# Kernel tuning notes

Hardware: AMD Instinct MI355X
Metric: run time of the kernel (lower is better)

The kernel has to match this reference:

```python
import jax, jax.numpy as jnp
import numpy as np

B, N = 16, 4096
N_IN, E_OUT = 128, 128          # inpt_dim[1], outp_dim[0]
OUT_N = 128                     # outp_dim[1]
G_DIM, CTXT_DIM = 64, 64
NODE_IN = E_OUT + N_IN          # 256, pre_ln size
CTXT_IN = G_DIM + CTXT_DIM      # 128
HID_F, HID_A = 256, 128
N_HEADS = 4
HEAD_DIM = OUT_N // N_HEADS     # 32
LN_EPS = 1e-5


def _init_w(key, fan_in, fan_out):
    return jax.random.normal(key, (fan_in, fan_out), jnp.float32) / np.float32(np.sqrt(fan_in))


def setup_inputs() -> dict:
    key = jax.random.key(0)
    ks = jax.random.split(key, 10)
    nodes = jax.random.normal(ks[0], (B, N, N_IN), jnp.float32)
    pooled_edges = jax.random.normal(ks[1], (B, N, E_OUT), jnp.float32)
    # variable-length graphs: valid prefix per graph (at least half the nodes)
    lengths = jax.random.randint(ks[2], (B,), N // 2, N + 1)
    mask = jnp.arange(N)[None, :] < lengths[:, None]
    globs = jax.random.normal(ks[3], (B, G_DIM), jnp.float32)
    ctxt = jax.random.normal(ks[4], (B, CTXT_DIM), jnp.float32)
    return {
        "nodes": nodes,
        "pooled_edges": pooled_edges,
        "mask": mask,
        "globs": globs,
        "ctxt": ctxt,
        "ln_g": jnp.ones((NODE_IN,), jnp.float32),
        "ln_b": jnp.zeros((NODE_IN,), jnp.float32),
        "feat_w1": _init_w(ks[5], NODE_IN + CTXT_IN, HID_F),
        "feat_b1": jnp.zeros((HID_F,), jnp.float32),
        "feat_w2": _init_w(ks[6], HID_F, OUT_N),
        "feat_b2": jnp.zeros((OUT_N,), jnp.float32),
        "attn_w1": _init_w(ks[7], NODE_IN + CTXT_IN, HID_A),
        "attn_b1": jnp.zeros((HID_A,), jnp.float32),
        "attn_w2": _init_w(ks[8], HID_A, N_HEADS),
        "attn_b2": jnp.zeros((N_HEADS,), jnp.float32),
    }


def _mlp(x, w1, b1, w2, b2):
    # DenseNetwork: one hidden block with LeakyReLU ("lrlu"), linear output
    h = jax.nn.leaky_relu(x @ w1 + b1)
    return h @ w2 + b2


def reference(nodes, pooled_edges, mask, globs, ctxt, ln_g, ln_b,
              feat_w1, feat_b1, feat_w2, feat_b2,
              attn_w1, attn_b1, attn_w2, attn_b2):
    # nodes = cat([graph.nodes, pooled_edges]) -> pre-LayerNorm
    x = jnp.concatenate([nodes, pooled_edges], axis=-1)           # [B,N,256]
    mu = jnp.mean(x, axis=-1, keepdims=True)
    var = jnp.var(x, axis=-1, keepdims=True)
    x = (x - mu) * jax.lax.rsqrt(var + LN_EPS) * ln_g + ln_b

    # high-level context broadcast to every node
    hl = jnp.concatenate([globs, ctxt], axis=-1)                   # [B,128]
    hl = jnp.broadcast_to(hl[:, None, :], (x.shape[0], x.shape[1], hl.shape[-1]))
    xin = jnp.concatenate([x, hl], axis=-1)                        # [B,N,384]

    # attention net with -inf padding, softmax over node axis (dim=-2)
    logits = _mlp(xin, attn_w1, attn_b1, attn_w2, attn_b2)          # [B,N,H]
    logits = jnp.where(mask[..., None], logits, -jnp.inf)
    w = jax.nn.softmax(logits, axis=1) / np.float32(np.sqrt(OUT_N))
    w = jnp.where(mask[..., None], w, 0.0)

    # feature net with 0 padding + residual (same_size)
    feats = _mlp(xin, feat_w1, feat_b1, feat_w2, feat_b2)           # [B,N,128]
    feats = jnp.where(mask[..., None], feats, 0.0)
    new_nodes = feats + nodes

    # expand per-head weights across head_dim, flatten, weighted node pooling
    w_full = jnp.repeat(w, HEAD_DIM, axis=-1)                       # [B,N,128]
    pooled = jnp.sum(new_nodes * w_full, axis=1)                    # [B,128]
    return (new_nodes, pooled)
```

## Files before the change

kernel.cpp:

```cpp
#include <hip/hip_runtime.h>
#include <stdint.h>

typedef unsigned short u16;
typedef unsigned char  u8;
typedef unsigned int   u32;
typedef __attribute__((ext_vector_type(8))) short bf16x8;
typedef __attribute__((ext_vector_type(4))) float f32x4;

static __device__ __forceinline__ float bf2f(u32 u) {
    union { u32 i; float f; } x; x.i = u << 16; return x.f;
}
static __device__ __forceinline__ u16 f2bf(float f) {
    union { u32 i; float f; } x; x.f = f;
    return (u16)((x.i + 0x7fffu + ((x.i >> 16) & 1u)) >> 16);
}
static __device__ __forceinline__ u32 packbf(float a, float b) {
    return (u32)f2bf(a) | ((u32)f2bf(b) << 16);
}
static __device__ __forceinline__ float ldf(const void* p, int i, int isf32) {
    return isf32 ? ((const float*)p)[i] : bf2f(((const u16*)p)[i]);
}
static __device__ __forceinline__ bool mvalid(const void* mask, int g, int mi32) {
    return mi32 ? (((const int*)mask)[g] != 0) : (((const u8*)mask)[g] != 0);
}

#define NTOT 65536
#define SXLD 264
#define SHLD 136

#define BAR() do { asm volatile("s_waitcnt lgkmcnt(0)" ::: "memory"); \
                   __builtin_amdgcn_s_barrier();                      \
                   asm volatile("" ::: "memory"); } while (0)

__global__ __launch_bounds__(256) void k0_prep(
    const void* __restrict__ feat_w1, const void* __restrict__ attn_w1,
    const void* __restrict__ feat_b1, const void* __restrict__ attn_b1,
    const void* __restrict__ feat_w2, const void* __restrict__ attn_w2,
    const void* __restrict__ globs, const void* __restrict__ ctxt,
    const void* __restrict__ ln_g,
    u16* __restrict__ W1t, u16* __restrict__ W2t, u16* __restrict__ aw2t,
    float* __restrict__ hlc)
{
    __shared__ u16 tile[64][66];
    __shared__ float hl[128];
    const int isf32 = (((const u32*)ln_g)[0] == 0x3F800000u);
    const int bid = blockIdx.x;
    const int t = threadIdx.x;

    if (bid < 24) {
        int jt = bid >> 2, kt = bid & 3;
        int j0 = jt * 64, k0 = kt * 64;
        int jj = t & 63, kq = t >> 6;
#pragma unroll
        for (int r = 0; r < 16; r++) {
            int kk = r * 4 + kq;
            int j = j0 + jj;
            float v = (j < 256) ? ldf(feat_w1, (k0 + kk) * 256 + j, isf32)
                                : ldf(attn_w1, (k0 + kk) * 128 + (j - 256), isf32);
            tile[kk][jj] = f2bf(v);
        }
        __syncthreads();
        int kk2 = t & 63, jq = t >> 6;
#pragma unroll
        for (int r = 0; r < 16; r++) {
            int jj2 = r * 4 + jq;
            W1t[(size_t)(j0 + jj2) * 256 + k0 + kk2] = tile[kk2][jj2];
        }
    } else if (bid < 32) {
        int id2 = bid - 24;
        int ct2 = id2 >> 2, kt = id2 & 3;
        int c0 = ct2 * 64, k0 = kt * 64;
        int cc = t & 63, kq = t >> 6;
#pragma unroll
        for (int r = 0; r < 16; r++) {
            int kk = r * 4 + kq;
            tile[kk][cc] = f2bf(ldf(feat_w2, (k0 + kk) * 128 + c0 + cc, isf32));
        }
        __syncthreads();
        int kk2 = t & 63, cq = t >> 6;
#pragma unroll
        for (int r = 0; r < 16; r++) {
            int cc2 = r * 4 + cq;
            W2t[(size_t)(c0 + cc2) * 256 + k0 + kk2] = tile[kk2][cc2];
        }
    } else if (bid == 32) {
#pragma unroll
        for (int i = 0; i < 8; i++) {
            int e = i * 256 + t;
            int n = e >> 7, k = e & 127;
            aw2t[e] = (n < 4) ? f2bf(ldf(attn_w2, k * 4 + n, isf32)) : (u16)0;
        }
    } else {
        int b = bid - 33;
        if (t < 64)       hl[t] = ldf(globs, b * 64 + t, isf32);
        else if (t < 128) hl[t] = ldf(ctxt, b * 64 + (t - 64), isf32);
        __syncthreads();
        {
            float s = ldf(feat_b1, t, isf32);
#pragma unroll 8
            for (int c = 0; c < 128; c++)
                s += hl[c] * ldf(feat_w1, (256 + c) * 256 + t, isf32);
            hlc[b * 384 + t] = s;
        }
        if (t < 128) {
            float s = ldf(attn_b1, t, isf32);
#pragma unroll 8
            for (int c = 0; c < 128; c++)
                s += hl[c] * ldf(attn_w1, (256 + c) * 128 + t, isf32);
            hlc[b * 384 + 256 + t] = s;
        }
    }
}

__global__ __launch_bounds__(256, 4) void k_mega(
    const void* __restrict__ nodes, const void* __restrict__ edges,
    const void* __restrict__ ln_g, const void* __restrict__ ln_b,
    const u16* __restrict__ W1t, const u16* __restrict__ W2t,
    const u16* __restrict__ aw2t, const float* __restrict__ hlc,
    const void* __restrict__ attn_b2, const void* __restrict__ feat_b2,
    const void* __restrict__ mask,
    float* __restrict__ logits, void* __restrict__ outp)
{
    __shared__ __align__(16) u16 sX[32 * SXLD];
    __shared__ __align__(16) u16 sH[2][32 * SHLD];
    __shared__ float sG[256], sBt[256];
    const int t = threadIdx.x;
    const int isf32 = (((const u32*)ln_g)[0] == 0x3F800000u);
    const int mi32  = (((const u32*)mask)[0] == 1u);
    const int r = t >> 3, q8 = t & 7;
    const int g00 = blockIdx.x * 64;
    const int g01 = g00 + 32;

    sG[t]  = ldf(ln_g, t, isf32);
    sBt[t] = ldf(ln_b, t, isf32);

    float4 f0a[4], f0b[4], f1a[4];
    uint4  u0[4],  u1[4];
    if (isf32) {
#pragma unroll
        for (int j = 0; j < 4; j++) {
            int c = q8 + j * 8;
            const float* s0 = (c < 16)
                ? ((const float*)nodes + (size_t)(g00 + r) * 128 + c * 8)
                : ((const float*)edges + (size_t)(g00 + r) * 128 + (c - 16) * 8);
            f0a[j] = ((const float4*)s0)[0];
            f0b[j] = ((const float4*)s0)[1];
        }
#pragma unroll
        for (int j = 0; j < 4; j++) {
            int c = q8 + j * 8;
            const float* s1 = (c < 16)
                ? ((const float*)nodes + (size_t)(g01 + r) * 128 + c * 8)
                : ((const float*)edges + (size_t)(g01 + r) * 128 + (c - 16) * 8);
            f1a[j] = ((const float4*)s1)[0];
        }
    } else {
#pragma unroll
        for (int j = 0; j < 4; j++) {
            int c = q8 + j * 8;
            const u16* s0 = (c < 16)
                ? ((const u16*)nodes + (size_t)(g00 + r) * 128 + c * 8)
                : ((const u16*)edges + (size_t)(g00 + r) * 128 + (c - 16) * 8);
            u0[j] = ((const uint4*)s0)[0];
        }
#pragma unroll
        for (int j = 0; j < 4; j++) {
            int c = q8 + j * 8;
            const u16* s1 = (c < 16)
                ? ((const u16*)nodes + (size_t)(g01 + r) * 128 + c * 8)
                : ((const u16*)edges + (size_t)(g01 + r) * 128 + (c - 16) * 8);
            u1[j] = ((const uint4*)s1)[0];
        }
    }
    BAR();

    u32 pk[16];

    auto ln_to_sX = [&]() {
        float s = 0.f, q = 0.f;
#pragma unroll
        for (int i = 0; i < 16; i++) {
            float lo = bf2f(pk[i] & 0xffffu), hi = bf2f(pk[i] >> 16);
            s += lo + hi; q += lo * lo + hi * hi;
        }
        s += __shfl_xor(s, 1, 64); s += __shfl_xor(s, 2, 64); s += __shfl_xor(s, 4, 64);
        q += __shfl_xor(q, 1, 64); q += __shfl_xor(q, 2, 64); q += __shfl_xor(q, 4, 64);
        float mu = s * (1.f / 256.f);
        float var = q * (1.f / 256.f) - mu * mu;
        float rs = rsqrtf(var + 1e-5f);
#pragma unroll
        for (int j = 0; j < 4; j++) {
            int c = q8 + j * 8;
            u32 ow[4];
#pragma unroll
            for (int k2 = 0; k2 < 4; k2++) {
                int col = c * 8 + k2 * 2;
                u32 w2 = pk[4 * j + k2];
                float y0 = (bf2f(w2 & 0xffffu) - mu) * rs * sG[col]     + sBt[col];
                float y1 = (bf2f(w2 >> 16)     - mu) * rs * sG[col + 1] + sBt[col + 1];
                ow[k2] = packbf(y0, y1);
            }
            *(uint4*)&sX[r * SXLD + c * 8] = make_uint4(ow[0], ow[1], ow[2], ow[3]);
        }
    };

    if (isf32) {
#pragma unroll
        for (int j = 0; j < 4; j++) {
            pk[4 * j]     = packbf(f0a[j].x, f0a[j].y);
            pk[4 * j + 1] = packbf(f0a[j].z, f0a[j].w);
            pk[4 * j + 2] = packbf(f0b[j].x, f0b[j].y);
            pk[4 * j + 3] = packbf(f0b[j].z, f0b[j].w);
        }
    } else {
#pragma unroll
        for (int j = 0; j < 4; j++) {
            pk[4 * j] = u0[j].x; pk[4 * j + 1] = u0[j].y;
            pk[4 * j + 2] = u0[j].z; pk[4 * j + 3] = u0[j].w;
        }
    }
    ln_to_sX();
    BAR();

    const int w = t >> 6, l = t & 63;
    const int lr = l & 15, lq = l >> 4;

    auto do_tile = [&](int g0) {
        const int b = g0 >> 12;
        f32x4 acc2[2][2];
#pragma unroll
        for (int rt = 0; rt < 2; rt++)
#pragma unroll
            for (int ct = 0; ct < 2; ct++) acc2[rt][ct] = (f32x4){0.f, 0.f, 0.f, 0.f};

        const int order[3] = {2, 0, 1};
#pragma unroll
        for (int oi = 0; oi < 3; oi++) {
            const int nt = order[oi];
            u16* sHc = &sH[oi & 1][0];

            float hbv[2];
#pragma unroll
            for (int ct = 0; ct < 2; ct++)
                hbv[ct] = hlc[b * 384 + nt * 128 + w * 32 + ct * 16 + lr];

            f32x4 acc1[2][2];
#pragma unroll
            for (int rt = 0; rt < 2; rt++)
#pragma unroll
                for (int ct = 0; ct < 2; ct++) acc1[rt][ct] = (f32x4){0.f, 0.f, 0.f, 0.f};

            const u16* Wp = W1t + (size_t)(nt * 128 + w * 32 + lr) * 256;
#pragma unroll
            for (int kh = 0; kh < 2; kh++) {
                bf16x8 bW[4][2];
#pragma unroll
                for (int kk = 0; kk < 4; kk++)
#pragma unroll
                    for (int ct = 0; ct < 2; ct++)
                        bW[kk][ct] = *(const bf16x8*)(Wp + ct * 16 * 256 + (kh * 4 + kk) * 32 + lq * 8);
#pragma unroll
                for (int kk = 0; kk < 4; kk++) {
                    bf16x8 aF[2];
#pragma unroll
                    for (int rt = 0; rt < 2; rt++)
                        aF[rt] = *(const bf16x8*)&sX[(rt * 16 + lr) * SXLD + ((kh * 4 + kk) * 4 + lq) * 8];
#pragma unroll
                    for (int rt = 0; rt < 2; rt++)
#pragma unroll
                        for (int ct = 0; ct < 2; ct++)
                            acc1[rt][ct] = __builtin_amdgcn_mfma_f32_16x16x32_bf16(aF[rt], bW[kk][ct], acc1[rt][ct], 0, 0, 0);
                }
            }

#pragma unroll
            for (int rt = 0; rt < 2; rt++)
#pragma unroll
                for (int ct = 0; ct < 2; ct++)
#pragma unroll
                    for (int reg = 0; reg < 4; reg++) {
                        int row = rt * 16 + lq * 4 + reg;
                        int col = w * 32 + ct * 16 + lr;
                        float hv = acc1[rt][ct][reg] + hbv[ct];
                        hv = (hv >= 0.f) ? hv : 0.01f * hv;
                        sHc[row * SHLD + col] = f2bf(hv);
                    }
            BAR();

            if (nt == 2) {
                if (w < 2) {
                    f32x4 accL = (f32x4){0.f, 0.f, 0.f, 0.f};
#pragma unroll
                    for (int kk = 0; kk < 4; kk++) {
                        bf16x8 aF = *(const bf16x8*)&sHc[(w * 16 + lr) * SHLD + (kk * 4 + lq) * 8];
                        bf16x8 bF = *(const bf16x8*)(aw2t + lr * 128 + kk * 32 + lq * 8);
                        accL = __builtin_amdgcn_mfma_f32_16x16x32_bf16(aF, bF, accL, 0, 0, 0);
                    }
                    if (lr < 4) {
                        float bias = ldf(attn_b2, lr, isf32);
#pragma unroll
                        for (int reg = 0; reg < 4; reg++) {
                            int row = g0 + w * 16 + lq * 4 + reg;
                            logits[(size_t)lr * NTOT + row] = accL[reg] + bias;
                        }
                    }
                }
            } else {
                const u16* W2p = W2t + (size_t)(w * 32 + lr) * 256 + nt * 128;
                bf16x8 bW2[4][2];
#pragma unroll
                for (int kk = 0; kk < 4; kk++)
#pragma unroll
                    for (int ct = 0; ct < 2; ct++)
                        bW2[kk][ct] = *(const bf16x8*)(W2p + ct * 16 * 256 + kk * 32 + lq * 8);
#pragma unroll
                for (int kk = 0; kk < 4; kk++) {
                    bf16x8 aF[2];
#pragma unroll
                    for (int rt = 0; rt < 2; rt++)
                        aF[rt] = *(const bf16x8*)&sHc[(rt * 16 + lr) * SHLD + (kk * 4 + lq) * 8];
#pragma unroll
                    for (int rt = 0; rt < 2; rt++)
#pragma unroll
                        for (int ct = 0; ct < 2; ct++)
                            acc2[rt][ct] = __builtin_amdgcn_mfma_f32_16x16x32_bf16(aF[rt], bW2[kk][ct], acc2[rt][ct], 0, 0, 0);
                }
            }
        }

#pragma unroll
        for (int rt = 0; rt < 2; rt++)
#pragma unroll
            for (int ct = 0; ct < 2; ct++)
#pragma unroll
                for (int reg = 0; reg < 4; reg++) {
                    int row = rt * 16 + lq * 4 + reg;
                    int col = w * 32 + ct * 16 + lr;
                    int g = g0 + row;
                    float v = acc2[rt][ct][reg] + ldf(feat_b2, col, isf32);
                    v = mvalid(mask, g, mi32) ? v : 0.f;
                    v += ldf(nodes, g * 128 + col, isf32);
                    size_t idx = (size_t)g * 128 + col;
                    if (isf32) ((float*)outp)[idx] = v;
                    else       ((u16*)outp)[idx] = f2bf(v);
                }
    };

    do_tile(g00);

    if (isf32) {
#pragma unroll
        for (int j = 0; j < 4; j++) {
            int c = q8 + j * 8;
            const float* s1 = (c < 16)
                ? ((const float*)nodes + (size_t)(g01 + r) * 128 + c * 8)
                : ((const float*)edges + (size_t)(g01 + r) * 128 + (c - 16) * 8);
            float4 fb = ((const float4*)s1)[1];
            pk[4 * j]     = packbf(f1a[j].x, f1a[j].y);
            pk[4 * j + 1] = packbf(f1a[j].z, f1a[j].w);
            pk[4 * j + 2] = packbf(fb.x, fb.y);
            pk[4 * j + 3] = packbf(fb.z, fb.w);
        }
    } else {
#pragma unroll
        for (int j = 0; j < 4; j++) {
            pk[4 * j] = u1[j].x; pk[4 * j + 1] = u1[j].y;
            pk[4 * j + 2] = u1[j].z; pk[4 * j + 3] = u1[j].w;
        }
    }
    ln_to_sX();
    BAR();

    do_tile(g01);
}

__global__ __launch_bounds__(1024) void k_softmax(
    const float* __restrict__ logits, const void* __restrict__ mask,
    const void* __restrict__ ln_g,
    float* __restrict__ wbuf, float* __restrict__ pooled)
{
    __shared__ float red[32];
    const int bh = blockIdx.x;
    const int b = bh >> 2, h = bh & 3;
    const int t = threadIdx.x;
    const int mi32 = (((const u32*)mask)[0] == 1u);
    if (t < 32) pooled[bh * 32 + t] = 0.f;

    float4 lg = ((const float4*)(logits + (size_t)h * NTOT + b * 4096))[t];
    int v0, v1, v2, v3;
    if (mi32) {
        int4 m4 = ((const int4*)mask)[b * 1024 + t];
        v0 = m4.x; v1 = m4.y; v2 = m4.z; v3 = m4.w;
    } else {
        u32 mb = ((const u32*)mask)[b * 1024 + t];
        v0 = mb & 255; v1 = (mb >> 8) & 255; v2 = (mb >> 16) & 255; v3 = mb >> 24;
    }
    float mx = -1e30f;
    if (v0) mx = lg.x;
    if (v1) mx = fmaxf(mx, lg.y);
    if (v2) mx = fmaxf(mx, lg.z);
    if (v3) mx = fmaxf(mx, lg.w);
#pragma unroll
    for (int o = 1; o < 64; o <<= 1) mx = fmaxf(mx, __shfl_xor(mx, o, 64));
    if ((t & 63) == 0) red[t >> 6] = mx;
    __syncthreads();
    float m2 = red[0];
#pragma unroll
    for (int i = 1; i < 16; i++) m2 = fmaxf(m2, red[i]);
    float e0 = v0 ? expf(lg.x - m2) : 0.f;
    float e1 = v1 ? expf(lg.y - m2) : 0.f;
    float e2 = v2 ? expf(lg.z - m2) : 0.f;
    float e3 = v3 ? expf(lg.w - m2) : 0.f;
    float sv = e0 + e1 + e2 + e3;
#pragma unroll
    for (int o = 1; o < 64; o <<= 1) sv += __shfl_xor(sv, o, 64);
    __syncthreads();
    if ((t & 63) == 0) red[16 + (t >> 6)] = sv;
    __syncthreads();
    float s2 = 0.f;
#pragma unroll
    for (int i = 0; i < 16; i++) s2 += red[16 + i];
    float inv = 0.08838834764831845f / s2;
    float4 o4 = make_float4(e0 * inv, e1 * inv, e2 * inv, e3 * inv);
    ((float4*)(wbuf + (size_t)h * NTOT + b * 4096))[t] = o4;
}

__global__ __launch_bounds__(256) void k_pool(
    const void* __restrict__ outp, const float* __restrict__ wbuf,
    const void* __restrict__ ln_g, float* __restrict__ pooled)
{
    __shared__ float sW[4][32];
    __shared__ float pacc[8][128];
    const int blk = blockIdx.x;
    const int b = blk >> 7, s = blk & 127;
    const int t = threadIdx.x;
    const int isf32 = (((const u32*)ln_g)[0] == 0x3F800000u);

    if (t < 128) {
        int h = t >> 5, n = t & 31;
        sW[h][n] = wbuf[(size_t)h * NTOT + b * 4096 + s * 32 + n];
    }
    __syncthreads();

    const int c4 = (t & 31) * 4, r8 = t >> 5;
    const int h = c4 >> 5;
    const size_t rowbase = (size_t)(b * 4096 + s * 32);
    float a0 = 0.f, a1 = 0.f, a2 = 0.f, a3 = 0.f;
    if (isf32) {
        const float* op = (const float*)outp;
#pragma unroll
        for (int i = 0; i < 4; i++) {
            int row = i * 8 + r8;
            float4 v = *(const float4*)(op + (rowbase + row) * 128 + c4);
            float wv = sW[h][row];
            a0 += v.x * wv; a1 += v.y * wv; a2 += v.z * wv; a3 += v.w * wv;
        }
    } else {
        const u16* op = (const u16*)outp;
#pragma unroll
        for (int i = 0; i < 4; i++) {
            int row = i * 8 + r8;
            uint2 v = *(const uint2*)(op + (rowbase + row) * 128 + c4);
            float wv = sW[h][row];
            a0 += bf2f(v.x & 0xffffu) * wv; a1 += bf2f(v.x >> 16) * wv;
            a2 += bf2f(v.y & 0xffffu) * wv; a3 += bf2f(v.y >> 16) * wv;
        }
    }
    *(float4*)&pacc[r8][c4] = make_float4(a0, a1, a2, a3);
    __syncthreads();
    if (t < 128) {
        float sum = 0.f;
#pragma unroll
        for (int r = 0; r < 8; r++) sum += pacc[r][t];
        atomicAdd(&pooled[b * 128 + t], sum);
    }
}

__global__ __launch_bounds__(256) void k_fin(const float* __restrict__ pooled,
                                             const void* __restrict__ ln_g,
                                             void* __restrict__ outbase)
{
    int t = blockIdx.x * 256 + threadIdx.x;
    const int isf32 = (((const u32*)ln_g)[0] == 0x3F800000u);
    if (t < 2048) {
        size_t off = (size_t)NTOT * 128 + t;
        if (isf32) ((float*)outbase)[off] = pooled[t];
        else       ((u16*)outbase)[off] = f2bf(pooled[t]);
    }
}

extern "C" void kernel_launch(void* const* d_in, const int* in_sizes, int n_in,
                              void* d_out, int out_size, void* d_ws, size_t ws_size,
                              hipStream_t stream)
{
    const void* nodes   = d_in[0];
    const void* edges   = d_in[1];
    const void* mask    = d_in[2];
    const void* globs   = d_in[3];
    const void* ctxt    = d_in[4];
    const void* ln_g    = d_in[5];
    const void* ln_b    = d_in[6];
    const void* feat_w1 = d_in[7];
    const void* feat_b1 = d_in[8];
    const void* feat_w2 = d_in[9];
    const void* feat_b2 = d_in[10];
    const void* attn_w1 = d_in[11];
    const void* attn_b1 = d_in[12];
    const void* attn_w2 = d_in[13];
    const void* attn_b2 = d_in[14];

    char* ws = (char*)d_ws;
    u16*   W1t    = (u16*)ws;   ws += (size_t)384 * 256 * 2;
    u16*   W2t    = (u16*)ws;   ws += (size_t)128 * 256 * 2;
    u16*   aw2t   = (u16*)ws;   ws += (size_t)16 * 128 * 2;
    float* hlc    = (float*)ws; ws += (size_t)16 * 384 * 4;
    float* logits = (float*)ws; ws += (size_t)NTOT * 4 * 4;
    float* wbuf   = (float*)ws; ws += (size_t)NTOT * 4 * 4;
    float* pooled = (float*)ws; ws += (size_t)2048 * 4;

    k0_prep  <<<dim3(49),   dim3(256),  0, stream>>>(feat_w1, attn_w1, feat_b1, attn_b1,
                                                     feat_w2, attn_w2, globs, ctxt, ln_g,
                                                     W1t, W2t, aw2t, hlc);
    k_mega   <<<dim3(1024), dim3(256),  0, stream>>>(nodes, edges, ln_g, ln_b, W1t, W2t,
                                                     aw2t, hlc, attn_b2, feat_b2, mask,
                                                     logits, d_out);
    k_softmax<<<dim3(64),   dim3(1024), 0, stream>>>(logits, mask, ln_g, wbuf, pooled);
    k_pool   <<<dim3(2048), dim3(256),  0, stream>>>(d_out, wbuf, ln_g, pooled);
    k_fin    <<<dim3(8),    dim3(256),  0, stream>>>(pooled, ln_g, d_out);
}
```

Baseline: 242.1 us.

## Stage feature-MLP output through LDS for coalesced residual add and stores

The epilogue now writes the MFMA accumulators plus bias into an LDS tile that reuses the sX buffer, then each thread reads back whole row segments. It adds the residual from node values already held in registers and writes vectorised, coalesced float4/uint4 stores, replacing scattered per-element global loads and stores. Mask validity and the output biases are hoisted out of the tile loop, and the second tile's node/edge loads are restructured so node values can be reused for the residual. This costs extra LDS traffic, extra barriers and more live registers, which could reduce occupancy.

```diff
diff --git a/kernel.cpp b/kernel.cpp
--- a/kernel.cpp
+++ b/kernel.cpp
@@ -27,6 +27,7 @@
 #define NTOT 65536
 #define SXLD 264
 #define SHLD 136
+#define SFLD 132
 
 #define BAR() do { asm volatile("s_waitcnt lgkmcnt(0)" ::: "memory"); \
                    __builtin_amdgcn_s_barrier();                      \
@@ -130,12 +131,15 @@
     const int r = t >> 3, q8 = t & 7;
     const int g00 = blockIdx.x * 64;
     const int g01 = g00 + 32;
+    float* sF = (float*)&sX[0];
 
     sG[t]  = ldf(ln_g, t, isf32);
     sBt[t] = ldf(ln_b, t, isf32);
 
-    float4 f0a[4], f0b[4], f1a[4];
-    uint4  u0[4],  u1[4];
+    float4 fa[4], fb[4];
+    float4 n1a0, n1b0, n1a1, n1b1;
+    uint4  ua[4];
+    uint4  un0, un1;
     if (isf32) {
 #pragma unroll
         for (int j = 0; j < 4; j++) {
@@ -143,17 +147,13 @@
             const float* s0 = (c < 16)
                 ? ((const float*)nodes + (size_t)(g00 + r) * 128 + c * 8)
                 : ((const float*)edges + (size_t)(g00 + r) * 128 + (c - 16) * 8);
-            f0a[j] = ((const float4*)s0)[0];
-            f0b[j] = ((const float4*)s0)[1];
-        }
-#pragma unroll
-        for (int j = 0; j < 4; j++) {
-            int c = q8 + j * 8;
-            const float* s1 = (c < 16)
-                ? ((const float*)nodes + (size_t)(g01 + r) * 128 + c * 8)
-                : ((const float*)edges + (size_t)(g01 + r) * 128 + (c - 16) * 8);
-            f1a[j] = ((const float4*)s1)[0];
-        }
+            fa[j] = ((const float4*)s0)[0];
+            fb[j] = ((const float4*)s0)[1];
+        }
+        const float* s1 = (const float*)nodes + (size_t)(g01 + r) * 128 + q8 * 8;
+        n1a0 = ((const float4*)s1)[0];  n1b0 = ((const float4*)s1)[1];
+        const float* s2 = s1 + 64;
+        n1a1 = ((const float4*)s2)[0];  n1b1 = ((const float4*)s2)[1];
     } else {
 #pragma unroll
         for (int j = 0; j < 4; j++) {
@@ -161,17 +161,14 @@
             const u16* s0 = (c < 16)
                 ? ((const u16*)nodes + (size_t)(g00 + r) * 128 + c * 8)
                 : ((const u16*)edges + (size_t)(g00 + r) * 128 + (c - 16) * 8);
-            u0[j] = ((const uint4*)s0)[0];
-        }
-#pragma unroll
-        for (int j = 0; j < 4; j++) {
-            int c = q8 + j * 8;
-            const u16* s1 = (c < 16)
-                ? ((const u16*)nodes + (size_t)(g01 + r) * 128 + c * 8)
-                : ((const u16*)edges + (size_t)(g01 + r) * 128 + (c - 16) * 8);
-            u1[j] = ((const uint4*)s1)[0];
-        }
-    }
+            ua[j] = ((const uint4*)s0)[0];
+        }
+        const u16* s1 = (const u16*)nodes + (size_t)(g01 + r) * 128 + q8 * 8;
+        un0 = ((const uint4*)s1)[0];
+        un1 = ((const uint4*)(s1 + 64))[0];
+    }
+    const bool mv0 = mvalid(mask, g00 + r, mi32);
+    const bool mv1 = mvalid(mask, g01 + r, mi32);
     BAR();
 
     u32 pk[16];
@@ -207,16 +204,16 @@
     if (isf32) {
 #pragma unroll
         for (int j = 0; j < 4; j++) {
-            pk[4 * j]     = packbf(f0a[j].x, f0a[j].y);
-            pk[4 * j + 1] = packbf(f0a[j].z, f0a[j].w);
-            pk[4 * j + 2] = packbf(f0b[j].x, f0b[j].y);
-            pk[4 * j + 3] = packbf(f0b[j].z, f0b[j].w);
+            pk[4 * j]     = packbf(fa[j].x, fa[j].y);
+            pk[4 * j + 1] = packbf(fa[j].z, fa[j].w);
+            pk[4 * j + 2] = packbf(fb[j].x, fb[j].y);
+            pk[4 * j + 3] = packbf(fb[j].z, fb[j].w);
         }
     } else {
 #pragma unroll
         for (int j = 0; j < 4; j++) {
-            pk[4 * j] = u0[j].x; pk[4 * j + 1] = u0[j].y;
-            pk[4 * j + 2] = u0[j].z; pk[4 * j + 3] = u0[j].w;
+            pk[4 * j] = ua[j].x; pk[4 * j + 1] = ua[j].y;
+            pk[4 * j + 2] = ua[j].z; pk[4 * j + 3] = ua[j].w;
         }
     }
     ln_to_sX();
@@ -224,8 +221,13 @@
 
     const int w = t >> 6, l = t & 63;
     const int lr = l & 15, lq = l >> 4;
-
-    auto do_tile = [&](int g0) {
+    const float fb2_0 = ldf(feat_b2, w * 32 + lr, isf32);
+    const float fb2_1 = ldf(feat_b2, w * 32 + 16 + lr, isf32);
+    const float ab2   = (lr < 4) ? ldf(attn_b2, lr, isf32) : 0.f;
+
+    auto do_tile = [&](int g0, bool mv,
+                       float4 na0, float4 nb0, float4 na1, float4 nb1,
+                       uint4 nu0, uint4 nu1) {
         const int b = g0 >> 12;
         f32x4 acc2[2][2];
 #pragma unroll
@@ -297,11 +299,10 @@
                         accL = __builtin_amdgcn_mfma_f32_16x16x32_bf16(aF, bF, accL, 0, 0, 0);
                     }
                     if (lr < 4) {
-                        float bias = ldf(attn_b2, lr, isf32);
 #pragma unroll
                         for (int reg = 0; reg < 4; reg++) {
                             int row = g0 + w * 16 + lq * 4 + reg;
-                            logits[(size_t)lr * NTOT + row] = accL[reg] + bias;
+                            logits[(size_t)lr * NTOT + row] = accL[reg] + ab2;
                         }
                     }
                 }
@@ -331,47 +332,87 @@
 #pragma unroll
         for (int rt = 0; rt < 2; rt++)
 #pragma unroll
-            for (int ct = 0; ct < 2; ct++)
+            for (int ct = 0; ct < 2; ct++) {
+                float fb2v = ct ? fb2_1 : fb2_0;
 #pragma unroll
                 for (int reg = 0; reg < 4; reg++) {
                     int row = rt * 16 + lq * 4 + reg;
                     int col = w * 32 + ct * 16 + lr;
-                    int g = g0 + row;
-                    float v = acc2[rt][ct][reg] + ldf(feat_b2, col, isf32);
-                    v = mvalid(mask, g, mi32) ? v : 0.f;
-                    v += ldf(nodes, g * 128 + col, isf32);
-                    size_t idx = (size_t)g * 128 + col;
-                    if (isf32) ((float*)outp)[idx] = v;
-                    else       ((u16*)outp)[idx] = f2bf(v);
+                    sF[row * SFLD + col] = acc2[rt][ct][reg] + fb2v;
                 }
+            }
+        BAR();
+
+        if (isf32) {
+            float* op = (float*)outp + (size_t)(g0 + r) * 128 + q8 * 8;
+            float4 v0 = *(float4*)&sF[r * SFLD + q8 * 8];
+            float4 v1 = *(float4*)&sF[r * SFLD + q8 * 8 + 4];
+            float4 v2 = *(float4*)&sF[r * SFLD + (q8 + 8) * 8];
+            float4 v3 = *(float4*)&sF[r * SFLD + (q8 + 8) * 8 + 4];
+            if (!mv) { v0 = v1 = v2 = v3 = make_float4(0.f, 0.f, 0.f, 0.f); }
+            v0.x += na0.x; v0.y += na0.y; v0.z += na0.z; v0.w += na0.w;
+            v1.x += nb0.x; v1.y += nb0.y; v1.z += nb0.z; v1.w += nb0.w;
+            v2.x += na1.x; v2.y += na1.y; v2.z += na1.z; v2.w += na1.w;
+            v3.x += nb1.x; v3.y += nb1.y; v3.z += nb1.z; v3.w += nb1.w;
+            ((float4*)op)[0] = v0;
+            ((float4*)op)[1] = v1;
+            ((float4*)(op + 64))[0] = v2;
+            ((float4*)(op + 64))[1] = v3;
+        } else {
+            u16* op = (u16*)outp + (size_t)(g0 + r) * 128 + q8 * 8;
+            float e[16];
+#pragma unroll
+            for (int i = 0; i < 8; i++) e[i]     = sF[r * SFLD + q8 * 8 + i];
+#pragma unroll
+            for (int i = 0; i < 8; i++) e[8 + i] = sF[r * SFLD + (q8 + 8) * 8 + i];
+            if (!mv) {
+#pragma unroll
+                for (int i = 0; i < 16; i++) e[i] = 0.f;
+            }
+            u32 nw[8] = {nu0.x, nu0.y, nu0.z, nu0.w, nu1.x, nu1.y, nu1.z, nu1.w};
+            u32 ow[8];
+#pragma unroll
+            for (int i = 0; i < 8; i++) {
+                float r0 = e[2 * i]     + bf2f(nw[i] & 0xffffu);
+                float r1 = e[2 * i + 1] + bf2f(nw[i] >> 16);
+                ow[i] = packbf(r0, r1);
+            }
+            ((uint4*)op)[0]        = make_uint4(ow[0], ow[1], ow[2], ow[3]);
+            ((uint4*)(op + 64))[0] = make_uint4(ow[4], ow[5], ow[6], ow[7]);
+        }
     };
 
-    do_tile(g00);
+    do_tile(g00, mv0, fa[0], fb[0], fa[1], fb[1], ua[0], ua[1]);
+
+    BAR();
 
     if (isf32) {
-#pragma unroll
-        for (int j = 0; j < 4; j++) {
-            int c = q8 + j * 8;
-            const float* s1 = (c < 16)
-                ? ((const float*)nodes + (size_t)(g01 + r) * 128 + c * 8)
-                : ((const float*)edges + (size_t)(g01 + r) * 128 + (c - 16) * 8);
-            float4 fb = ((const float4*)s1)[1];
-            pk[4 * j]     = packbf(f1a[j].x, f1a[j].y);
-            pk[4 * j + 1] = packbf(f1a[j].z, f1a[j].w);
-            pk[4 * j + 2] = packbf(fb.x, fb.y);
-            pk[4 * j + 3] = packbf(fb.z, fb.w);
-        }
+        const float* s2 = (const float*)edges + (size_t)(g01 + r) * 128 + q8 * 8;
+        float4 e2a = ((const float4*)s2)[0];
+        float4 e2b = ((const float4*)s2)[1];
+        float4 e3a = ((const float4*)(s2 + 64))[0];
+        float4 e3b = ((const float4*)(s2 + 64))[1];
+        pk[0] = packbf(n1a0.x, n1a0.y); pk[1] = packbf(n1a0.z, n1a0.w);
+        pk[2] = packbf(n1b0.x, n1b0.y); pk[3] = packbf(n1b0.z, n1b0.w);
+        pk[4] = packbf(n1a1.x, n1a1.y); pk[5] = packbf(n1a1.z, n1a1.w);
+        pk[6] = packbf(n1b1.x, n1b1.y); pk[7] = packbf(n1b1.z, n1b1.w);
+        pk[8]  = packbf(e2a.x, e2a.y); pk[9]  = packbf(e2a.z, e2a.w);
+        pk[10] = packbf(e2b.x, e2b.y); pk[11] = packbf(e2b.z, e2b.w);
+        pk[12] = packbf(e3a.x, e3a.y); pk[13] = packbf(e3a.z, e3a.w);
+        pk[14] = packbf(e3b.x, e3b.y); pk[15] = packbf(e3b.z, e3b.w);
     } else {
-#pragma unroll
-        for (int j = 0; j < 4; j++) {
-            pk[4 * j] = u1[j].x; pk[4 * j + 1] = u1[j].y;
-            pk[4 * j + 2] = u1[j].z; pk[4 * j + 3] = u1[j].w;
-        }
+        const u16* s2 = (const u16*)edges + (size_t)(g01 + r) * 128 + q8 * 8;
+        uint4 ue2 = ((const uint4*)s2)[0];
+        uint4 ue3 = ((const uint4*)(s2 + 64))[0];
+        pk[0] = un0.x; pk[1] = un0.y; pk[2] = un0.z; pk[3] = un0.w;
+        pk[4] = un1.x; pk[5] = un1.y; pk[6] = un1.z; pk[7] = un1.w;
+        pk[8]  = ue2.x; pk[9]  = ue2.y; pk[10] = ue2.z; pk[11] = ue2.w;
+        pk[12] = ue3.x; pk[13] = ue3.y; pk[14] = ue3.z; pk[15] = ue3.w;
     }
     ln_to_sX();
     BAR();
 
-    do_tile(g01);
+    do_tile(g01, mv1, n1a0, n1b0, n1a1, n1b1, un0, un1);
 }
 
 __global__ __launch_bounds__(1024) void k_softmax(
```

Measured after the change: 242.8 us. Within noise of the previous version (+0.3%).
